# Kernel tuning notes

Measured on AMD Instinct MI355X. Metric: run time of the kernel, lower is better.

## Reference

```python
import jax, jax.numpy as jnp
import numpy as np

B, C, H, W = 4, 64, 96, 96
HEAD_SIZE = 4


def setup_inputs() -> dict:
    key = jax.random.key(0)
    ks = jax.random.split(key, 9)
    s = 1.0 / np.sqrt(C)
    d = {"x": jax.random.normal(ks[0], (B, C, H, W), dtype=jnp.float32)}
    for i, name in enumerate(["Wq", "Wk", "Wv", "Wo"]):
        d[name] = jax.random.normal(ks[1 + i], (C, C), dtype=jnp.float32) * s
    for i, name in enumerate(["bq", "bk", "bv", "bo"]):
        d[name] = jax.random.normal(ks[5 + i], (C,), dtype=jnp.float32) * 0.01
    return d


def reference(x, Wq, bq, Wk, bk, Wv, bv, Wo, bo):
    b, c, h, w = x.shape
    hw = h * w
    hs = HEAD_SIZE
    S = hw // hs  # spatial tokens per head (heads split along HW, not channels)
    scale = 1.0 / jnp.sqrt(jnp.asarray(hs, x.dtype))

    def proj(y, Wm, bias):  # 1x1 conv == per-pixel channel matmul
        return jnp.einsum('bchw,oc->bohw', y, Wm) + bias[None, :, None, None]

    def heads(y):  # (B,C,H,W) -> (B,hs,C,S)
        return y.reshape(b, c, hs, S).transpose(0, 2, 1, 3)

    q = heads(proj(x, Wq, bq))  # (B,hs,C,S)
    k = heads(proj(x, Wk, bk))  # (B,hs,C,S)
    v = heads(proj(x, Wv, bv))  # (B,hs,C,S)

    # attention = softmax(q^T k / sqrt(head_size)) over last axis: (B,hs,S,S)
    attn = jax.nn.softmax(jnp.einsum('bhcs,bhct->bhst', q, k) * scale, axis=-1)
    # out = v @ attn^T : (B,hs,C,S)
    out = jnp.einsum('bhcs,bhts->bhct', v, attn)
    # torch .reshape on the (B,hs,C,S) layout -> (B,C,H,W); jnp.reshape matches
    out = out.reshape(b, c, h, w)
    out = jnp.einsum('bchw,oc->bohw', out, Wo) + bo[None, :, None, None]
    return x + out
```

## Files before the change

kernel.cpp:

```cpp
#include <hip/hip_runtime.h>
#include <stdint.h>

#define HW_  9216
#define S_   2304
#define NBH  16
#define NSPLIT 4
#define JPS  9
#define NPART ((size_t)NBH * S_ * 64)
#define SCALE_LOG2E 0.72134752044448169136f

using f32x4 = __attribute__((ext_vector_type(4))) float;
using u32x4 = __attribute__((ext_vector_type(4))) uint32_t;
using u32x2 = __attribute__((ext_vector_type(2))) uint32_t;
using s16x8 = __attribute__((ext_vector_type(8))) short;

typedef const __attribute__((address_space(1))) void gbl_void;
typedef __attribute__((address_space(3))) void lds_void;

__device__ __forceinline__ uint32_t pkbf(float lo, float hi) {
    uint32_t r;
    asm("v_cvt_pk_bf16_f32 %0, %1, %2" : "=v"(r) : "v"(lo), "v"(hi));
    return r;
}
__device__ __forceinline__ float bf2f(uint16_t h) {
    return __builtin_bit_cast(float, (uint32_t)h << 16);
}

__global__ __launch_bounds__(192) void qkv_fused(
    const float* __restrict__ x,
    const float* __restrict__ Wq, const float* __restrict__ Wk, const float* __restrict__ Wv,
    const float* __restrict__ bq, const float* __restrict__ bk, const float* __restrict__ bv,
    uint16_t* __restrict__ Qo, uint16_t* __restrict__ Ko, uint16_t* __restrict__ Vo)
{
    const int pix0 = blockIdx.x * 64;
    const int b   = pix0 / HW_;
    const int hw0 = pix0 % HW_;
    const int h   = hw0 / S_;
    const int s0  = hw0 % S_;
    const int bh  = b * 4 + h;

    const int tid  = threadIdx.x;
    const int wave = tid >> 6;
    const int lane = tid & 63;
    const int g = lane >> 4, lr = lane & 15;

    __shared__ alignas(16) uint16_t xt[64 * 64];

    {
        const float* xb = x + (size_t)b * 64 * HW_ + hw0 + lane;
        const int cb_begin = wave * 3;
        const int cb_end   = (wave == 2) ? 8 : wave * 3 + 3;
        for (int cb = cb_begin; cb < cb_end; ++cb) {
            uint32_t rp[4];
            #pragma unroll
            for (int e = 0; e < 4; ++e)
                rp[e] = pkbf(xb[(size_t)(cb * 8 + 2 * e) * HW_],
                             xb[(size_t)(cb * 8 + 2 * e + 1) * HW_]);
            u32x4 d = { rp[0], rp[1], rp[2], rp[3] };
            *(u32x4*)(xt + lane * 64 + 8 * (cb ^ (lane & 7))) = d;
        }
    }
    __syncthreads();

    const float* W    = (wave == 0) ? Wq : (wave == 1) ? Wk : Wv;
    const float* bias = (wave == 0) ? bq : (wave == 1) ? bk : bv;
    const float ws = (wave == 0) ? SCALE_LOG2E : 1.0f;

    s16x8 wf[4][2];
    #pragma unroll
    for (int t4 = 0; t4 < 4; ++t4)
        #pragma unroll
        for (int ks = 0; ks < 2; ++ks) {
            const float* wp = W + (t4 * 16 + lr) * 64 + ks * 32 + g * 8;
            f32x4 w0 = *(const f32x4*)wp;
            f32x4 w1 = *(const f32x4*)(wp + 4);
            u32x4 d = { pkbf(w0[0] * ws, w0[1] * ws), pkbf(w0[2] * ws, w0[3] * ws),
                        pkbf(w1[0] * ws, w1[1] * ws), pkbf(w1[2] * ws, w1[3] * ws) };
            wf[t4][ks] = __builtin_bit_cast(s16x8, d);
        }

    s16x8 xf[4][2];
    #pragma unroll
    for (int pt = 0; pt < 4; ++pt)
        #pragma unroll
        for (int ks = 0; ks < 2; ++ks) {
            const int pix = pt * 16 + lr;
            xf[pt][ks] = *(const s16x8*)(xt + pix * 64 + 8 * ((ks * 4 + g) ^ (pix & 7)));
        }

    if (wave != 2) {
        f32x4 acc[4][4];
        #pragma unroll
        for (int mt = 0; mt < 4; ++mt) {
            f32x4 bi = *(const f32x4*)(bias + mt * 16 + g * 4);
            bi *= ws;
            #pragma unroll
            for (int nt = 0; nt < 4; ++nt) acc[mt][nt] = bi;
        }
        #pragma unroll
        for (int ks = 0; ks < 2; ++ks)
            #pragma unroll
            for (int mt = 0; mt < 4; ++mt)
                #pragma unroll
                for (int nt = 0; nt < 4; ++nt)
                    acc[mt][nt] = __builtin_amdgcn_mfma_f32_16x16x32_bf16(
                        wf[mt][ks], xf[nt][ks], acc[mt][nt], 0, 0, 0);
        uint16_t* dst = ((wave == 0) ? Qo : Ko) + ((size_t)bh * S_ + s0) * 64;
        #pragma unroll
        for (int mt = 0; mt < 4; ++mt)
            #pragma unroll
            for (int nt = 0; nt < 4; ++nt) {
                uint32_t d0 = pkbf(acc[mt][nt][0], acc[mt][nt][1]);
                uint32_t d1 = pkbf(acc[mt][nt][2], acc[mt][nt][3]);
                const int o = mt * 16 + g * 4;
                *(uint32_t*)(dst + (nt * 16 + lr) * 64 + o)     = d0;
                *(uint32_t*)(dst + (nt * 16 + lr) * 64 + o + 2) = d1;
            }
    } else {
        f32x4 acc[4][4];
        #pragma unroll
        for (int nt = 0; nt < 4; ++nt) {
            const float bv = bias[nt * 16 + lr];
            #pragma unroll
            for (int mt = 0; mt < 4; ++mt) acc[mt][nt] = (f32x4){bv, bv, bv, bv};
        }
        #pragma unroll
        for (int ks = 0; ks < 2; ++ks)
            #pragma unroll
            for (int mt = 0; mt < 4; ++mt)
                #pragma unroll
                for (int nt = 0; nt < 4; ++nt)
                    acc[mt][nt] = __builtin_amdgcn_mfma_f32_16x16x32_bf16(
                        xf[mt][ks], wf[nt][ks], acc[mt][nt], 0, 0, 0);
        uint16_t* dst = Vo + (size_t)bh * 64 * S_;
        #pragma unroll
        for (int mt = 0; mt < 4; ++mt)
            #pragma unroll
            for (int nt = 0; nt < 4; ++nt) {
                uint32_t d0 = pkbf(acc[mt][nt][0], acc[mt][nt][1]);
                uint32_t d1 = pkbf(acc[mt][nt][2], acc[mt][nt][3]);
                const int o = nt * 16 + lr;
                const int sb = s0 + mt * 16 + g * 4;
                *(uint32_t*)(dst + (size_t)o * S_ + sb)     = d0;
                *(uint32_t*)(dst + (size_t)o * S_ + sb + 2) = d1;
            }
    }
}

__global__ __launch_bounds__(256, 4) void attn(
    const uint16_t* __restrict__ Qg, const uint16_t* __restrict__ Kg,
    const uint16_t* __restrict__ Vg, uint16_t* __restrict__ Op,
    float* __restrict__ Lp)
{
    const int blk = blockIdx.x;
    const int xcd = blk & 7;
    const int i   = blk >> 3;
    const int bh  = xcd * 2 + (i & 1);
    const int i2  = i >> 1;
    const int sp  = i2 & 3;
    const int qb  = i2 >> 2;
    const int j0  = sp * JPS;
    const int b   = bh >> 2;
    const int h   = bh & 3;

    const int tid  = threadIdx.x;
    const int wave = tid >> 6;
    const int lane = tid & 63;
    const int g    = lane >> 4;
    const int lr   = lane & 15;
    const int q0   = qb * 128 + wave * 32;

    __shared__ alignas(16) uint16_t Kl[4096];
    __shared__ alignas(16) uint16_t Vl[4096];
    __shared__ alignas(16) uint16_t Pw[4][2304];
    uint16_t* P = Pw[wave];

    const uint16_t* Qb = Qg + (size_t)bh * S_ * 64;
    const uint16_t* Kb = Kg + (size_t)bh * S_ * 64;
    const uint16_t* Vb = Vg + (size_t)bh * 64 * S_;

    s16x8 qf[2][2];
    #pragma unroll
    for (int qt = 0; qt < 2; ++qt)
        #pragma unroll
        for (int ks = 0; ks < 2; ++ks)
            qf[qt][ks] = *(const s16x8*)(Qb + (size_t)(q0 + qt * 16 + lr) * 64 + ks * 32 + g * 8);

    f32x4 oacc[2][4];
    float l_r[2][4];
    #pragma unroll
    for (int qt = 0; qt < 2; ++qt) {
        #pragma unroll
        for (int ct = 0; ct < 4; ++ct) oacc[qt][ct] = (f32x4){0.f, 0.f, 0.f, 0.f};
        #pragma unroll
        for (int r = 0; r < 4; ++r) l_r[qt][r] = 0.f;
    }

    for (int jj = 0; jj < JPS; ++jj) {
        const int j = j0 + jj;
        #pragma unroll
        for (int call = 0; call < 2; ++call) {
            const int chunk = wave * 128 + call * 64 + lane;
            const int row   = chunk >> 3;
            const int cb    = (chunk & 7) ^ (row & 7);
            __builtin_amdgcn_global_load_lds(
                (gbl_void*)(Kb + ((size_t)(j * 64 + row) * 64 + cb * 8)),
                (lds_void*)(Kl + (wave * 128 + call * 64) * 8), 16, 0, 0);
            __builtin_amdgcn_global_load_lds(
                (gbl_void*)(Vb + ((size_t)row * S_ + j * 64 + cb * 8)),
                (lds_void*)(Vl + (wave * 128 + call * 64) * 8), 16, 0, 0);
        }
        asm volatile("s_waitcnt vmcnt(0)" ::: "memory");
        __syncthreads();

        f32x4 sacc[2][4];
        #pragma unroll
        for (int qt = 0; qt < 2; ++qt)
            #pragma unroll
            for (int kt = 0; kt < 4; ++kt) sacc[qt][kt] = (f32x4){0.f, 0.f, 0.f, 0.f};
        #pragma unroll
        for (int ks = 0; ks < 2; ++ks)
            #pragma unroll
            for (int kt = 0; kt < 4; ++kt) {
                const int key = kt * 16 + lr;
                s16x8 kf = *(const s16x8*)(&Kl[key * 64 + 8 * ((ks * 4 + g) ^ (key & 7))]);
                sacc[0][kt] = __builtin_amdgcn_mfma_f32_16x16x32_bf16(qf[0][ks], kf, sacc[0][kt], 0, 0, 0);
                sacc[1][kt] = __builtin_amdgcn_mfma_f32_16x16x32_bf16(qf[1][ks], kf, sacc[1][kt], 0, 0, 0);
            }

        #pragma unroll
        for (int qt = 0; qt < 2; ++qt)
            #pragma unroll
            for (int kt = 0; kt < 4; ++kt)
                #pragma unroll
                for (int r = 0; r < 4; ++r) {
                    const float pv = __builtin_amdgcn_exp2f(sacc[qt][kt][r]);
                    l_r[qt][r] += pv;
                    P[(qt * 16 + 4 * g + r) * 72 + kt * 16 + lr] = (uint16_t)pkbf(pv, pv);
                }

        #pragma unroll
        for (int ks = 0; ks < 2; ++ks) {
            s16x8 pf0 = *(const s16x8*)(P + (0 * 16 + lr) * 72 + ks * 32 + g * 8);
            s16x8 pf1 = *(const s16x8*)(P + (1 * 16 + lr) * 72 + ks * 32 + g * 8);
            #pragma unroll
            for (int ct = 0; ct < 4; ++ct) {
                const int c = ct * 16 + lr;
                s16x8 vf = *(const s16x8*)(&Vl[c * 64 + 8 * ((ks * 4 + g) ^ (c & 7))]);
                oacc[0][ct] = __builtin_amdgcn_mfma_f32_16x16x32_bf16(pf0, vf, oacc[0][ct], 0, 0, 0);
                oacc[1][ct] = __builtin_amdgcn_mfma_f32_16x16x32_bf16(pf1, vf, oacc[1][ct], 0, 0, 0);
            }
        }

        __syncthreads();
    }

    #pragma unroll
    for (int mask = 1; mask < 16; mask <<= 1) {
        #pragma unroll
        for (int qt = 0; qt < 2; ++qt)
            #pragma unroll
            for (int r = 0; r < 4; ++r)
                l_r[qt][r] += __shfl_xor(l_r[qt][r], mask, 64);
    }

    #pragma unroll
    for (int qt = 0; qt < 2; ++qt)
        #pragma unroll
        for (int ct = 0; ct < 4; ++ct) {
            uint32_t d0 = pkbf(oacc[qt][ct][0], oacc[qt][ct][1]);
            uint32_t d1 = pkbf(oacc[qt][ct][2], oacc[qt][ct][3]);
            const int base = (ct * 16 + lr) * 36 + qt * 16 + 4 * g;
            *(uint32_t*)(P + base)     = d0;
            *(uint32_t*)(P + base + 2) = d1;
        }
    __syncthreads();

    const int c = lane;
    u32x2 wv[8];
    #pragma unroll
    for (int e = 0; e < 8; ++e)
        wv[e] = *(const u32x2*)(P + c * 36 + e * 4);
    uint16_t* dst = Op + (size_t)sp * NPART
                  + ((size_t)(b * 64 + h * 16 + (c >> 2)) * HW_ + (c & 3) * S_ + q0);
    #pragma unroll
    for (int s4 = 0; s4 < 4; ++s4) {
        u32x4 d = { wv[2 * s4][0], wv[2 * s4][1], wv[2 * s4 + 1][0], wv[2 * s4 + 1][1] };
        *(u32x4*)(dst + s4 * 8) = d;
    }

    if (lr == 0) {
        #pragma unroll
        for (int qt = 0; qt < 2; ++qt)
            #pragma unroll
            for (int r = 0; r < 4; ++r)
                Lp[((size_t)sp * NBH + bh) * S_ + q0 + qt * 16 + 4 * g + r] = l_r[qt][r];
    }
}

__global__ __launch_bounds__(128) void out_proj(
    const uint16_t* __restrict__ Op, const float* __restrict__ Lp,
    const float* __restrict__ x,
    const float* __restrict__ Wo, const float* __restrict__ bo,
    float* __restrict__ out)
{
    const int pix0 = blockIdx.x * 64;
    const int b   = pix0 / HW_;
    const int hw0 = pix0 % HW_;
    const int tid  = threadIdx.x;
    const int wave = tid >> 6;
    const int lane = tid & 63;
    const int g = lane >> 4, lr = lane & 15;
    const int o0 = wave * 32;
    const int t = (hw0 % S_) + lane;

    __shared__ alignas(16) uint16_t at[64 * 64];

    float inv[4];
    #pragma unroll
    for (int hh = 0; hh < 4; ++hh) {
        float sl = 0.f;
        #pragma unroll
        for (int sp2 = 0; sp2 < NSPLIT; ++sp2)
            sl += Lp[((size_t)sp2 * NBH + b * 4 + hh) * S_ + t];
        inv[hh] = 1.0f / sl;
    }

    {
        const size_t base = (size_t)b * 64 * HW_ + hw0 + lane;
        #pragma unroll
        for (int cbi = 0; cbi < 4; ++cbi) {
            const int cb = wave * 4 + cbi;
            uint32_t rp[4];
            #pragma unroll
            for (int e = 0; e < 4; ++e) {
                const int cc = cb * 4 + e;
                float a0 = 0.f, a1 = 0.f;
                #pragma unroll
                for (int sp2 = 0; sp2 < NSPLIT; ++sp2) {
                    const size_t o2 = (size_t)sp2 * NPART + base;
                    a0 += bf2f(Op[o2 + (size_t)(2 * cc) * HW_]);
                    a1 += bf2f(Op[o2 + (size_t)(2 * cc + 1) * HW_]);
                }
                rp[e] = pkbf(a0 * inv[(2 * cc) >> 4], a1 * inv[(2 * cc + 1) >> 4]);
            }
            u32x4 d = { rp[0], rp[1], rp[2], rp[3] };
            *(u32x4*)(at + lane * 64 + 8 * (cb ^ (lane & 7))) = d;
        }
    }
    __syncthreads();

    s16x8 wf[2][2];
    #pragma unroll
    for (int t2 = 0; t2 < 2; ++t2)
        #pragma unroll
        for (int ks = 0; ks < 2; ++ks) {
            const float* wp = Wo + (o0 + t2 * 16 + lr) * 64 + ks * 32 + g * 8;
            f32x4 w0 = *(const f32x4*)wp;
            f32x4 w1 = *(const f32x4*)(wp + 4);
            u32x4 d = { pkbf(w0[0], w0[1]), pkbf(w0[2], w0[3]),
                        pkbf(w1[0], w1[1]), pkbf(w1[2], w1[3]) };
            wf[t2][ks] = __builtin_bit_cast(s16x8, d);
        }

    s16x8 af[4][2];
    #pragma unroll
    for (int pt = 0; pt < 4; ++pt)
        #pragma unroll
        for (int ks = 0; ks < 2; ++ks) {
            const int pix = pt * 16 + lr;
            af[pt][ks] = *(const s16x8*)(at + pix * 64 + 8 * ((ks * 4 + g) ^ (pix & 7)));
        }

    f32x4 acc[2][4];
    #pragma unroll
    for (int mt = 0; mt < 2; ++mt) {
        f32x4 bi = *(const f32x4*)(bo + o0 + mt * 16 + g * 4);
        #pragma unroll
        for (int nt = 0; nt < 4; ++nt) acc[mt][nt] = bi;
    }
    #pragma unroll
    for (int ks = 0; ks < 2; ++ks)
        #pragma unroll
        for (int mt = 0; mt < 2; ++mt)
            #pragma unroll
            for (int nt = 0; nt < 4; ++nt)
                acc[mt][nt] = __builtin_amdgcn_mfma_f32_16x16x32_bf16(
                    wf[mt][ks], af[nt][ks], acc[mt][nt], 0, 0, 0);

    #pragma unroll
    for (int mt = 0; mt < 2; ++mt)
        #pragma unroll
        for (int nt = 0; nt < 4; ++nt) {
            const int o = o0 + mt * 16 + g * 4;
            const size_t rowb = ((size_t)(b * 64 + o)) * HW_ + hw0 + nt * 16 + lr;
            #pragma unroll
            for (int r = 0; r < 4; ++r) {
                const size_t a2 = rowb + (size_t)r * HW_;
                out[a2] = acc[mt][nt][r] + x[a2];
            }
        }
}

extern "C" void kernel_launch(void* const* d_in, const int* in_sizes, int n_in,
                              void* d_out, int out_size, void* d_ws, size_t ws_size,
                              hipStream_t stream) {
    const float* x  = (const float*)d_in[0];
    const float* Wq = (const float*)d_in[1];
    const float* Wk = (const float*)d_in[2];
    const float* Wv = (const float*)d_in[3];
    const float* Wo = (const float*)d_in[4];
    const float* bq = (const float*)d_in[5];
    const float* bk = (const float*)d_in[6];
    const float* bv = (const float*)d_in[7];
    const float* bo = (const float*)d_in[8];
    float* out = (float*)d_out;

    uint16_t* Q  = (uint16_t*)d_ws;
    uint16_t* K  = Q + NPART;
    uint16_t* V  = K + NPART;
    uint16_t* Op = V + NPART;
    float*    Lp = (float*)(Op + (size_t)NSPLIT * NPART);

    qkv_fused<<<576, 192, 0, stream>>>(x, Wq, Wk, Wv, bq, bk, bv, Q, K, V);
    attn<<<1152, 256, 0, stream>>>(Q, K, V, Op, Lp);
    out_proj<<<576, 128, 0, stream>>>(Op, Lp, x, Wo, bo, out);
}
```

Measured before the change: 66.10 us.

## Use eight waves of 16 query rows each in attention blocks

The attention block doubles from 4 to 8 waves, and each wave now owns 16 query rows instead of 32. Every wave issues one K and one V LDS load per tile instead of two, and per-wave register and LDS footprints shrink. This should raise wave-level parallelism and occupancy and hide latency better. In exchange, each K/V fragment read from LDS is used by only one MFMA instead of two, so LDS read traffic per FLOP doubles, and the block-wide barrier now spans more waves.

```diff
diff --git a/kernel.cpp b/kernel.cpp
--- a/kernel.cpp
+++ b/kernel.cpp
@@ -147,7 +147,7 @@
     }
 }
 
-__global__ __launch_bounds__(256, 4) void attn(
+__global__ __launch_bounds__(512, 4) void attn(
     const uint16_t* __restrict__ Qg, const uint16_t* __restrict__ Kg,
     const uint16_t* __restrict__ Vg, uint16_t* __restrict__ Op,
     float* __restrict__ Lp)
@@ -168,87 +168,74 @@
     const int lane = tid & 63;
     const int g    = lane >> 4;
     const int lr   = lane & 15;
-    const int q0   = qb * 128 + wave * 32;
+    const int q0   = qb * 128 + wave * 16;
 
     __shared__ alignas(16) uint16_t Kl[4096];
     __shared__ alignas(16) uint16_t Vl[4096];
-    __shared__ alignas(16) uint16_t Pw[4][2304];
+    __shared__ alignas(16) uint16_t Pw[8][1280];
     uint16_t* P = Pw[wave];
 
     const uint16_t* Qb = Qg + (size_t)bh * S_ * 64;
     const uint16_t* Kb = Kg + (size_t)bh * S_ * 64;
     const uint16_t* Vb = Vg + (size_t)bh * 64 * S_;
 
-    s16x8 qf[2][2];
-    #pragma unroll
-    for (int qt = 0; qt < 2; ++qt)
-        #pragma unroll
-        for (int ks = 0; ks < 2; ++ks)
-            qf[qt][ks] = *(const s16x8*)(Qb + (size_t)(q0 + qt * 16 + lr) * 64 + ks * 32 + g * 8);
-
-    f32x4 oacc[2][4];
-    float l_r[2][4];
-    #pragma unroll
-    for (int qt = 0; qt < 2; ++qt) {
-        #pragma unroll
-        for (int ct = 0; ct < 4; ++ct) oacc[qt][ct] = (f32x4){0.f, 0.f, 0.f, 0.f};
-        #pragma unroll
-        for (int r = 0; r < 4; ++r) l_r[qt][r] = 0.f;
-    }
+    s16x8 qf[2];
+    #pragma unroll
+    for (int ks = 0; ks < 2; ++ks)
+        qf[ks] = *(const s16x8*)(Qb + (size_t)(q0 + lr) * 64 + ks * 32 + g * 8);
+
+    f32x4 oacc[4];
+    float l_r[4];
+    #pragma unroll
+    for (int ct = 0; ct < 4; ++ct) oacc[ct] = (f32x4){0.f, 0.f, 0.f, 0.f};
+    #pragma unroll
+    for (int r = 0; r < 4; ++r) l_r[r] = 0.f;
 
     for (int jj = 0; jj < JPS; ++jj) {
         const int j = j0 + jj;
-        #pragma unroll
-        for (int call = 0; call < 2; ++call) {
-            const int chunk = wave * 128 + call * 64 + lane;
+        {
+            const int chunk = wave * 64 + lane;
             const int row   = chunk >> 3;
             const int cb    = (chunk & 7) ^ (row & 7);
             __builtin_amdgcn_global_load_lds(
                 (gbl_void*)(Kb + ((size_t)(j * 64 + row) * 64 + cb * 8)),
-                (lds_void*)(Kl + (wave * 128 + call * 64) * 8), 16, 0, 0);
+                (lds_void*)(Kl + (wave * 64) * 8), 16, 0, 0);
             __builtin_amdgcn_global_load_lds(
                 (gbl_void*)(Vb + ((size_t)row * S_ + j * 64 + cb * 8)),
-                (lds_void*)(Vl + (wave * 128 + call * 64) * 8), 16, 0, 0);
+                (lds_void*)(Vl + (wave * 64) * 8), 16, 0, 0);
         }
         asm volatile("s_waitcnt vmcnt(0)" ::: "memory");
         __syncthreads();
 
-        f32x4 sacc[2][4];
-        #pragma unroll
-        for (int qt = 0; qt < 2; ++qt)
-            #pragma unroll
-            for (int kt = 0; kt < 4; ++kt) sacc[qt][kt] = (f32x4){0.f, 0.f, 0.f, 0.f};
+        f32x4 sacc[4];
+        #pragma unroll
+        for (int kt = 0; kt < 4; ++kt) sacc[kt] = (f32x4){0.f, 0.f, 0.f, 0.f};
         #pragma unroll
         for (int ks = 0; ks < 2; ++ks)
             #pragma unroll
             for (int kt = 0; kt < 4; ++kt) {
                 const int key = kt * 16 + lr;
                 s16x8 kf = *(const s16x8*)(&Kl[key * 64 + 8 * ((ks * 4 + g) ^ (key & 7))]);
-                sacc[0][kt] = __builtin_amdgcn_mfma_f32_16x16x32_bf16(qf[0][ks], kf, sacc[0][kt], 0, 0, 0);
-                sacc[1][kt] = __builtin_amdgcn_mfma_f32_16x16x32_bf16(qf[1][ks], kf, sacc[1][kt], 0, 0, 0);
-            }
-
-        #pragma unroll
-        for (int qt = 0; qt < 2; ++qt)
-            #pragma unroll
-            for (int kt = 0; kt < 4; ++kt)
-                #pragma unroll
-                for (int r = 0; r < 4; ++r) {
-                    const float pv = __builtin_amdgcn_exp2f(sacc[qt][kt][r]);
-                    l_r[qt][r] += pv;
-                    P[(qt * 16 + 4 * g + r) * 72 + kt * 16 + lr] = (uint16_t)pkbf(pv, pv);
-                }
+                sacc[kt] = __builtin_amdgcn_mfma_f32_16x16x32_bf16(qf[ks], kf, sacc[kt], 0, 0, 0);
+            }
+
+        #pragma unroll
+        for (int kt = 0; kt < 4; ++kt)
+            #pragma unroll
+            for (int r = 0; r < 4; ++r) {
+                const float pv = __builtin_amdgcn_exp2f(sacc[kt][r]);
+                l_r[r] += pv;
+                P[(4 * g + r) * 72 + kt * 16 + lr] = (uint16_t)pkbf(pv, pv);
+            }
 
         #pragma unroll
         for (int ks = 0; ks < 2; ++ks) {
-            s16x8 pf0 = *(const s16x8*)(P + (0 * 16 + lr) * 72 + ks * 32 + g * 8);
-            s16x8 pf1 = *(const s16x8*)(P + (1 * 16 + lr) * 72 + ks * 32 + g * 8);
+            s16x8 pf = *(const s16x8*)(P + lr * 72 + ks * 32 + g * 8);
             #pragma unroll
             for (int ct = 0; ct < 4; ++ct) {
                 const int c = ct * 16 + lr;
                 s16x8 vf = *(const s16x8*)(&Vl[c * 64 + 8 * ((ks * 4 + g) ^ (c & 7))]);
-                oacc[0][ct] = __builtin_amdgcn_mfma_f32_16x16x32_bf16(pf0, vf, oacc[0][ct], 0, 0, 0);
-                oacc[1][ct] = __builtin_amdgcn_mfma_f32_16x16x32_bf16(pf1, vf, oacc[1][ct], 0, 0, 0);
+                oacc[ct] = __builtin_amdgcn_mfma_f32_16x16x32_bf16(pf, vf, oacc[ct], 0, 0, 0);
             }
         }
 
@@ -258,43 +245,38 @@
     #pragma unroll
     for (int mask = 1; mask < 16; mask <<= 1) {
         #pragma unroll
-        for (int qt = 0; qt < 2; ++qt)
-            #pragma unroll
-            for (int r = 0; r < 4; ++r)
-                l_r[qt][r] += __shfl_xor(l_r[qt][r], mask, 64);
-    }
-
-    #pragma unroll
-    for (int qt = 0; qt < 2; ++qt)
-        #pragma unroll
-        for (int ct = 0; ct < 4; ++ct) {
-            uint32_t d0 = pkbf(oacc[qt][ct][0], oacc[qt][ct][1]);
-            uint32_t d1 = pkbf(oacc[qt][ct][2], oacc[qt][ct][3]);
-            const int base = (ct * 16 + lr) * 36 + qt * 16 + 4 * g;
-            *(uint32_t*)(P + base)     = d0;
-            *(uint32_t*)(P + base + 2) = d1;
-        }
+        for (int r = 0; r < 4; ++r)
+            l_r[r] += __shfl_xor(l_r[r], mask, 64);
+    }
+
+    #pragma unroll
+    for (int ct = 0; ct < 4; ++ct) {
+        uint32_t d0 = pkbf(oacc[ct][0], oacc[ct][1]);
+        uint32_t d1 = pkbf(oacc[ct][2], oacc[ct][3]);
+        const int base = (ct * 16 + lr) * 20 + 4 * g;
+        *(uint32_t*)(P + base)     = d0;
+        *(uint32_t*)(P + base + 2) = d1;
+    }
     __syncthreads();
 
     const int c = lane;
-    u32x2 wv[8];
-    #pragma unroll
-    for (int e = 0; e < 8; ++e)
-        wv[e] = *(const u32x2*)(P + c * 36 + e * 4);
+    u32x2 wv[4];
+    #pragma unroll
+    for (int e = 0; e < 4; ++e)
+        wv[e] = *(const u32x2*)(P + c * 20 + e * 4);
     uint16_t* dst = Op + (size_t)sp * NPART
                   + ((size_t)(b * 64 + h * 16 + (c >> 2)) * HW_ + (c & 3) * S_ + q0);
-    #pragma unroll
-    for (int s4 = 0; s4 < 4; ++s4) {
-        u32x4 d = { wv[2 * s4][0], wv[2 * s4][1], wv[2 * s4 + 1][0], wv[2 * s4 + 1][1] };
-        *(u32x4*)(dst + s4 * 8) = d;
+    {
+        u32x4 d0 = { wv[0][0], wv[0][1], wv[1][0], wv[1][1] };
+        u32x4 d1 = { wv[2][0], wv[2][1], wv[3][0], wv[3][1] };
+        *(u32x4*)(dst)     = d0;
+        *(u32x4*)(dst + 8) = d1;
     }
 
     if (lr == 0) {
         #pragma unroll
-        for (int qt = 0; qt < 2; ++qt)
-            #pragma unroll
-            for (int r = 0; r < 4; ++r)
-                Lp[((size_t)sp * NBH + bh) * S_ + q0 + qt * 16 + 4 * g + r] = l_r[qt][r];
+        for (int r = 0; r < 4; ++r)
+            Lp[((size_t)sp * NBH + bh) * S_ + q0 + 4 * g + r] = l_r[r];
     }
 }
 
@@ -423,6 +405,6 @@
     float*    Lp = (float*)(Op + (size_t)NSPLIT * NPART);
 
     qkv_fused<<<576, 192, 0, stream>>>(x, Wq, Wk, Wv, bq, bk, bv, Q, K, V);
-    attn<<<1152, 256, 0, stream>>>(Q, K, V, Op, Lp);
+    attn<<<1152, 512, 0, stream>>>(Q, K, V, Op, Lp);
     out_proj<<<576, 128, 0, stream>>>(Op, Lp, x, Wo, bo, out);
 }
```

Measured after the change: 66.03 us, median of 2. About the same (-0.1%).
